# Optimization experiments

Hardware: AMD Instinct MI355X
Metric: run time of the kernel (lower is better)

Reference implementation:

```python
import jax, jax.numpy as jnp
import numpy as np

B, S, F, H = 64, 1024, 64, 128


def setup_inputs() -> dict:
    key = jax.random.key(0)
    ks = jax.random.split(key, 12)
    s = 1.0 / np.sqrt(H)
    u = lambda k, shape: jax.random.uniform(k, shape, jnp.float32, -s, s)
    return {
        "x": jax.random.normal(ks[0], (B, S, F), jnp.float32),
        "mu": jax.random.normal(ks[1], (B, 1, F), jnp.float32),
        "W_ih0": u(ks[2], (4 * H, F)),
        "W_hh0": u(ks[3], (4 * H, H)),
        "b_ih0": u(ks[4], (4 * H,)),
        "b_hh0": u(ks[5], (4 * H,)),
        "W_ih1": u(ks[6], (4 * H, H)),
        "W_hh1": u(ks[7], (4 * H, H)),
        "b_ih1": u(ks[8], (4 * H,)),
        "b_hh1": u(ks[9], (4 * H,)),
        "fc_w": u(ks[10], (1, H)),
        "fc_b": u(ks[11], (1,)),
    }


def _cell(x_gates, h, c, Whh, bias):
    # PyTorch LSTM cell: gates ordered i, f, g, o
    g = x_gates + h @ Whh.T + bias
    i, f, gg, o = jnp.split(g, 4, axis=-1)
    c = jax.nn.sigmoid(f) * c + jax.nn.sigmoid(i) * jnp.tanh(gg)
    h = jax.nn.sigmoid(o) * jnp.tanh(c)
    return h, c


def _lstm2(x1, x2, Wih, Whh, bih, bhh):
    # 2-step LSTM layer from zero initial state; returns per-step hidden states
    bias = bih + bhh
    n = x1.shape[0]
    hd = Whh.shape[1]
    h0 = jnp.zeros((n, hd), x1.dtype)
    h1, c1 = _cell(x1 @ Wih.T, h0, h0, Whh, bias)
    h2, _ = _cell(x2 @ Wih.T, h1, c1, Whh, bias)
    return h1, h2


def reference(x, mu, W_ih0, W_hh0, b_ih0, b_hh0, W_ih1, W_hh1, b_ih1, b_hh1, fc_w, fc_b):
    b, s, f = x.shape
    # Every timestep runs an independent 2-step LSTM [x_t, mu] from zero state,
    # so fold (batch, seq) into one big batch of B*S instances.
    x1 = x.reshape(b * s, f)                                   # step-1 inputs
    x2 = jnp.broadcast_to(mu, (b, s, f)).reshape(b * s, f)     # step-2 inputs (mu)
    h1, h2 = _lstm2(x1, x2, W_ih0, W_hh0, b_ih0, b_hh0)        # layer 0
    _, h2 = _lstm2(h1, h2, W_ih1, W_hh1, b_ih1, b_hh1)         # layer 1
    h = jax.nn.relu(h2).reshape(b, s, -1)                      # relu; dropout is identity (eval)
    out = h @ fc_w.T + fc_b                                    # [B, S, 1]
    return out
```

## Files before the change

### kernel.cpp

```cpp
#include <hip/hip_runtime.h>


typedef _Float16 half8 __attribute__((ext_vector_type(8)));
typedef _Float16 half4_t __attribute__((ext_vector_type(4)));
typedef float f32x4 __attribute__((ext_vector_type(4)));

#define L2E  1.4426950408889634f
#define L2E2 2.8853900817779268f

#define WP_WIH0 0
#define WP_WHH0 32768
#define WP_WIH1 98304
#define WP_WHH1 163840
#define WS_BIAS0 458752
#define WS_BIAS1 (458752 + 2048)
#define WS_MUG2  (458752 + 4096)

__global__ void prep_kernel(const float* __restrict__ Wih0,
                            const float* __restrict__ Whh0,
                            const float* __restrict__ Wih1,
                            const float* __restrict__ Whh1,
                            const float* __restrict__ bih0,
                            const float* __restrict__ bhh0,
                            const float* __restrict__ bih1,
                            const float* __restrict__ bhh1,
                            const float* __restrict__ mu,
                            _Float16* __restrict__ Wp,
                            float* __restrict__ bias0f,
                            float* __restrict__ bias1f,
                            float* __restrict__ mu_g2)
{
    int blk = blockIdx.x;
    if (blk >= 113) {
        int o = (blk - 113) * 256 + threadIdx.x;
        int b = o >> 9;
        int n = o & 511;
        float s = bih0[n] + bhh0[n];
        const float* m = mu + b * 64;
        const float* wrow = Wih0 + n * 64;
        #pragma unroll 8
        for (int k = 0; k < 64; ++k) s += m[k] * wrow[k];
        float scale = ((n >> 7) == 2) ? L2E2 : L2E;
        mu_g2[o] = s * scale;
        return;
    }
    if (blk == 112) {
        int i = threadIdx.x;
        float sc_hi = (i < 128) ? L2E2 : L2E;
        bias0f[i]       = (bih0[i]       + bhh0[i])       * L2E;
        bias0f[i + 256] = (bih0[i + 256] + bhh0[i + 256]) * sc_hi;
        bias1f[i]       = (bih1[i]       + bhh1[i])       * L2E;
        bias1f[i + 256] = (bih1[i + 256] + bhh1[i + 256]) * sc_hi;
        return;
    }
    int gidx = blk * 256 + threadIdx.x;
    const float* src; int KC, Kw, local;
    if (gidx < 4096)       { src = Wih0; KC = 2; Kw = 64;  local = gidx; }
    else if (gidx < 12288) { src = Whh0; KC = 4; Kw = 128; local = gidx - 4096; }
    else if (gidx < 20480) { src = Wih1; KC = 4; Kw = 128; local = gidx - 12288; }
    else                   { src = Whh1; KC = 4; Kw = 128; local = gidx - 20480; }
    int lane = local & 63;
    int tmp  = local >> 6;
    int kc   = tmp % KC;
    int nt   = tmp / KC;
    int n  = nt * 16 + (lane & 15);
    int k0 = kc * 32 + (lane >> 4) * 8;
    float scale = ((n >> 7) == 2) ? L2E2 : L2E;
    const float* s = src + n * Kw + k0;
    half8 hv;
    #pragma unroll
    for (int j = 0; j < 8; ++j) hv[j] = (_Float16)(s[j] * scale);
    *(half8*)(Wp + (size_t)gidx * 8) = hv;
}

__device__ __forceinline__ float sig2(float a) {
    return __builtin_amdgcn_rcpf(1.0f + __builtin_amdgcn_exp2f(-a));
}
__device__ __forceinline__ float tanh2(float a) {
    return fmaf(-2.0f, __builtin_amdgcn_rcpf(1.0f + __builtin_amdgcn_exp2f(a)), 1.0f);
}

__device__ __forceinline__ int swz(int row, int col) {
    return (row << 8) + (col ^ ((row & 7) << 4));
}

template<int KC>
__device__ __forceinline__ void gemm_stage(const _Float16* __restrict__ Wq,
                                           const _Float16* A, const int strideA,
                                           int w, int lane, f32x4 acc[4][4])
{
    const int c = lane & 15, q = lane >> 4;
    #pragma unroll
    for (int kc = 0; kc < KC; ++kc) {
        half8 a[4], bq[4];
        #pragma unroll
        for (int mt = 0; mt < 4; ++mt)
            a[mt] = *(const half8*)(A + (mt * 16 + c) * strideA + kc * 32 + q * 8);
        #pragma unroll
        for (int g = 0; g < 4; ++g)
            bq[g] = *(const half8*)(Wq + (((g * 8 + w) * KC + kc) * 64 + lane) * 8);
        #pragma unroll
        for (int mt = 0; mt < 4; ++mt)
            #pragma unroll
            for (int g = 0; g < 4; ++g)
                acc[mt][g] = __builtin_amdgcn_mfma_f32_16x16x32_f16(bq[g], a[mt], acc[mt][g], 0, 0, 0);
    }
}

template<int KC>
__device__ __forceinline__ void gemm_lds(const _Float16* __restrict__ Wq,
                                         const char* Hb,
                                         int w, int lane, f32x4 acc[4][4])
{
    const int c = lane & 15, q = lane >> 4;
    #pragma unroll
    for (int kc = 0; kc < KC; ++kc) {
        half8 a[4], bq[4];
        #pragma unroll
        for (int mt = 0; mt < 4; ++mt)
            a[mt] = *(const half8*)(Hb + swz(mt * 16 + c, kc * 64 + q * 16));
        #pragma unroll
        for (int g = 0; g < 4; ++g)
            bq[g] = *(const half8*)(Wq + (((g * 8 + w) * KC + kc) * 64 + lane) * 8);
        #pragma unroll
        for (int mt = 0; mt < 4; ++mt)
            #pragma unroll
            for (int g = 0; g < 4; ++g)
                acc[mt][g] = __builtin_amdgcn_mfma_f32_16x16x32_f16(bq[g], a[mt], acc[mt][g], 0, 0, 0);
    }
}

__global__ __launch_bounds__(512) void lstm_main(
    const float* __restrict__ x, const _Float16* __restrict__ Wp_in,
    const float* __restrict__ bias0f_in, const float* __restrict__ bias1f_in,
    const float* __restrict__ mu_g2_in, const float* __restrict__ fc_w_in,
    const float* __restrict__ fc_b_in, float* __restrict__ out)
{
    __shared__ __align__(16) char smem[58368];
    char* H1s  = smem;
    char* H2s  = smem + 16384;
    char* H11s = smem + 32768;
    _Float16* A0 = (_Float16*)(smem + 49152);

    const int t = threadIdx.x;
    const int w = t >> 6, lane = t & 63, c = lane & 15, q = lane >> 4;
    const int wg = blockIdx.x;
    const int b = wg >> 4;
    const int bq_idx = w * 4 + q;

    {
        const float* xp = x + (size_t)wg * 4096 + t * 8;
        float4 u0 = ((const float4*)xp)[0];
        float4 u1 = ((const float4*)xp)[1];
        half8 hv;
        hv[0] = (_Float16)u0.x; hv[1] = (_Float16)u0.y;
        hv[2] = (_Float16)u0.z; hv[3] = (_Float16)u0.w;
        hv[4] = (_Float16)u1.x; hv[5] = (_Float16)u1.y;
        hv[6] = (_Float16)u1.z; hv[7] = (_Float16)u1.w;
        *(half8*)(A0 + (t >> 3) * 72 + (t & 7) * 8) = hv;
        if (t < 64) out[(size_t)wg * 64 + t] = fc_b_in[0];
    }
    __syncthreads();

    f32x4 acc[4][4];
    float cc[4][4];

    {
        const float* bias0f = bias0f_in; asm volatile("" : "+s"(bias0f));
        #pragma unroll
        for (int g = 0; g < 4; ++g) {
            f32x4 bv = ((const f32x4*)bias0f)[g * 32 + bq_idx];
            #pragma unroll
            for (int mt = 0; mt < 4; ++mt) acc[mt][g] = bv;
        }
    }
    {
        const _Float16* W0 = Wp_in + WP_WIH0; asm volatile("" : "+s"(W0));
        __builtin_amdgcn_s_setprio(1);
        gemm_stage<2>(W0, A0, 72, w, lane, acc);
        __builtin_amdgcn_s_setprio(0);
    }
    #pragma unroll
    for (int mt = 0; mt < 4; ++mt) {
        half4_t hv;
        #pragma unroll
        for (int r = 0; r < 4; ++r) {
            float c1 = sig2(acc[mt][0][r]) * tanh2(acc[mt][2][r]);
            cc[mt][r] = c1;
            hv[r] = (_Float16)(sig2(acc[mt][3][r]) * tanh2(c1 * L2E2));
        }
        *(half4_t*)(H1s + swz(mt * 16 + c, w * 32 + q * 8)) = hv;
    }
    __syncthreads();

    {
        const float* mu_g2b = mu_g2_in + b * 512; asm volatile("" : "+s"(mu_g2b));
        #pragma unroll
        for (int g = 0; g < 4; ++g) {
            f32x4 bv = ((const f32x4*)mu_g2b)[g * 32 + bq_idx];
            #pragma unroll
            for (int mt = 0; mt < 4; ++mt) acc[mt][g] = bv;
        }
    }
    {
        const _Float16* Wq = Wp_in + WP_WHH0; asm volatile("" : "+s"(Wq));
        __builtin_amdgcn_s_setprio(1);
        gemm_lds<4>(Wq, H1s, w, lane, acc);
        __builtin_amdgcn_s_setprio(0);
    }

    f32x4 bv1[4];
    {
        const float* bias1f = bias1f_in; asm volatile("" : "+s"(bias1f));
        #pragma unroll
        for (int g = 0; g < 4; ++g)
            bv1[g] = ((const f32x4*)bias1f)[g * 32 + bq_idx];
    }

    {
        const _Float16* Wih1p = Wp_in + WP_WIH1; asm volatile("" : "+s"(Wih1p));
        #pragma unroll
        for (int mt = 0; mt < 4; ++mt) {
            half4_t hv;
            #pragma unroll
            for (int r = 0; r < 4; ++r) {
                float c2 = sig2(acc[mt][1][r]) * cc[mt][r]
                         + sig2(acc[mt][0][r]) * tanh2(acc[mt][2][r]);
                hv[r] = (_Float16)(sig2(acc[mt][3][r]) * tanh2(c2 * L2E2));
            }
            *(half4_t*)(H2s + swz(mt * 16 + c, w * 32 + q * 8)) = hv;
            #pragma unroll
            for (int g = 0; g < 4; ++g) acc[mt][g] = bv1[g];
            __builtin_amdgcn_s_setprio(1);
            #pragma unroll
            for (int kc = 0; kc < 4; ++kc) {
                half8 av = *(const half8*)(H1s + swz(mt * 16 + c, kc * 64 + q * 16));
                #pragma unroll
                for (int g = 0; g < 4; ++g) {
                    half8 bq = *(const half8*)(Wih1p + (((g * 8 + w) * 4 + kc) * 64 + lane) * 8);
                    acc[mt][g] = __builtin_amdgcn_mfma_f32_16x16x32_f16(bq, av, acc[mt][g], 0, 0, 0);
                }
            }
            __builtin_amdgcn_s_setprio(0);
        }
    }
    #pragma unroll
    for (int mt = 0; mt < 4; ++mt) {
        half4_t hv;
        #pragma unroll
        for (int r = 0; r < 4; ++r) {
            float c1 = sig2(acc[mt][0][r]) * tanh2(acc[mt][2][r]);
            cc[mt][r] = c1;
            hv[r] = (_Float16)(sig2(acc[mt][3][r]) * tanh2(c1 * L2E2));
        }
        *(half4_t*)(H11s + swz(mt * 16 + c, w * 32 + q * 8)) = hv;
    }
    __syncthreads();

    #pragma unroll
    for (int g = 0; g < 4; ++g)
        #pragma unroll
        for (int mt = 0; mt < 4; ++mt) acc[mt][g] = bv1[g];
    {
        const _Float16* Wa = Wp_in + WP_WIH1; asm volatile("" : "+s"(Wa));
        const _Float16* Wb = Wp_in + WP_WHH1; asm volatile("" : "+s"(Wb));
        __builtin_amdgcn_s_setprio(1);
        gemm_lds<4>(Wa, H2s,  w, lane, acc);
        gemm_lds<4>(Wb, H11s, w, lane, acc);
        __builtin_amdgcn_s_setprio(0);
    }
    {
        const float* fc_w = fc_w_in; asm volatile("" : "+s"(fc_w));
        f32x4 fwv = ((const f32x4*)fc_w)[bq_idx];
        #pragma unroll
        for (int mt = 0; mt < 4; ++mt) {
            float v = 0.0f;
            #pragma unroll
            for (int r = 0; r < 4; ++r) {
                float c2 = sig2(acc[mt][1][r]) * cc[mt][r]
                         + sig2(acc[mt][0][r]) * tanh2(acc[mt][2][r]);
                float h  = sig2(acc[mt][3][r]) * tanh2(c2 * L2E2);
                v = fmaf(fmaxf(h, 0.0f), fwv[r], v);
            }
            v += __shfl_xor(v, 16);
            v += __shfl_xor(v, 32);
            if (lane < 16)
                atomicAdd(out + (size_t)wg * 64 + mt * 16 + lane, v);
        }
    }
}

extern "C" void kernel_launch(void* const* d_in, const int* in_sizes, int n_in,
                              void* d_out, int out_size, void* d_ws, size_t ws_size,
                              hipStream_t stream)
{
    const float* x    = (const float*)d_in[0];
    const float* mu   = (const float*)d_in[1];
    const float* Wih0 = (const float*)d_in[2];
    const float* Whh0 = (const float*)d_in[3];
    const float* bih0 = (const float*)d_in[4];
    const float* bhh0 = (const float*)d_in[5];
    const float* Wih1 = (const float*)d_in[6];
    const float* Whh1 = (const float*)d_in[7];
    const float* bih1 = (const float*)d_in[8];
    const float* bhh1 = (const float*)d_in[9];
    const float* fcw  = (const float*)d_in[10];
    const float* fcb  = (const float*)d_in[11];
    float* out = (float*)d_out;

    _Float16* Wp  = (_Float16*)d_ws;
    float* bias0f = (float*)((char*)d_ws + WS_BIAS0);
    float* bias1f = (float*)((char*)d_ws + WS_BIAS1);
    float* mu_g2  = (float*)((char*)d_ws + WS_MUG2);

    hipLaunchKernelGGL(prep_kernel, dim3(241), dim3(256), 0, stream,
                       Wih0, Whh0, Wih1, Whh1, bih0, bhh0, bih1, bhh1, mu,
                       Wp, bias0f, bias1f, mu_g2);
    hipLaunchKernelGGL(lstm_main, dim3(1024), dim3(512), 0, stream,
                       x, Wp, bias0f, bias1f, mu_g2, fcw, fcb, out);
}
```

Measured before the change: 144.7 us.

## Software-pipeline weight fragment loads across GEMM stages with lighter barriers

Merges the GEMM helpers into one routine that prefetches the next k-chunk's weight fragments into registers while the current MFMAs run, carrying the prefetch into the next stage's weights. It folds bias initialisation into the first MFMA's accumulator input and swaps __syncthreads for an LDS-only wait plus s_barrier. The layer-1 step-1 GEMM is moved out of the per-mt interleaving with the layer-0 activation write, so H2s is fully written before Wih1·H1 runs. These changes aim to hide global/L2 weight-load latency, at the cost of extra live registers that could lower occupancy or cause spills.

Result: faster. 134.7 us (-6.9%).

```diff
diff --git a/kernel.cpp b/kernel.cpp
--- a/kernel.cpp
+++ b/kernel.cpp
@@ -84,49 +84,60 @@
     return (row << 8) + (col ^ ((row & 7) << 4));
 }
 
-template<int KC>
-__device__ __forceinline__ void gemm_stage(const _Float16* __restrict__ Wq,
-                                           const _Float16* A, const int strideA,
-                                           int w, int lane, f32x4 acc[4][4])
+__device__ __forceinline__ void lds_barrier() {
+    asm volatile("s_waitcnt lgkmcnt(0)" ::: "memory");
+    __builtin_amdgcn_s_barrier();
+    asm volatile("" ::: "memory");
+}
+
+__device__ __forceinline__ void load_bq(half8 bq[4], const _Float16* __restrict__ Wq,
+                                        int KC, int kc, int w, int lane)
+{
+    #pragma unroll
+    for (int g = 0; g < 4; ++g)
+        bq[g] = *(const half8*)(Wq + (((g * 8 + w) * KC + kc) * 64 + lane) * 8);
+}
+
+template<int SRC>
+__device__ __forceinline__ void load_a(half8 a[4], const char* base, int kc, int c, int q)
+{
+    #pragma unroll
+    for (int mt = 0; mt < 4; ++mt) {
+        if (SRC == 0)
+            a[mt] = *(const half8*)((const _Float16*)base + (mt * 16 + c) * 72 + kc * 32 + q * 8);
+        else
+            a[mt] = *(const half8*)(base + swz(mt * 16 + c, kc * 64 + q * 16));
+    }
+}
+
+template<int KC, int SRC, bool PF, bool FIRST>
+__device__ __forceinline__ void gemm_pf(const _Float16* __restrict__ Wq,
+                                        const char* Abase,
+                                        const _Float16* __restrict__ Wnext, int KCnext,
+                                        half8 bqc[4], const f32x4 bv[4],
+                                        int w, int lane, f32x4 acc[4][4])
 {
     const int c = lane & 15, q = lane >> 4;
     #pragma unroll
     for (int kc = 0; kc < KC; ++kc) {
-        half8 a[4], bq[4];
+        half8 bqn[4];
+        if (kc + 1 < KC)  load_bq(bqn, Wq, KC, kc + 1, w, lane);
+        else if (PF)      load_bq(bqn, Wnext, KCnext, 0, w, lane);
+        half8 a[4];
+        load_a<SRC>(a, Abase, kc, c, q);
+        __builtin_amdgcn_s_setprio(1);
         #pragma unroll
         for (int mt = 0; mt < 4; ++mt)
-            a[mt] = *(const half8*)(A + (mt * 16 + c) * strideA + kc * 32 + q * 8);
-        #pragma unroll
-        for (int g = 0; g < 4; ++g)
-            bq[g] = *(const half8*)(Wq + (((g * 8 + w) * KC + kc) * 64 + lane) * 8);
-        #pragma unroll
-        for (int mt = 0; mt < 4; ++mt)
-            #pragma unroll
-            for (int g = 0; g < 4; ++g)
-                acc[mt][g] = __builtin_amdgcn_mfma_f32_16x16x32_f16(bq[g], a[mt], acc[mt][g], 0, 0, 0);
-    }
-}
-
-template<int KC>
-__device__ __forceinline__ void gemm_lds(const _Float16* __restrict__ Wq,
-                                         const char* Hb,
-                                         int w, int lane, f32x4 acc[4][4])
-{
-    const int c = lane & 15, q = lane >> 4;
-    #pragma unroll
-    for (int kc = 0; kc < KC; ++kc) {
-        half8 a[4], bq[4];
-        #pragma unroll
-        for (int mt = 0; mt < 4; ++mt)
-            a[mt] = *(const half8*)(Hb + swz(mt * 16 + c, kc * 64 + q * 16));
-        #pragma unroll
-        for (int g = 0; g < 4; ++g)
-            bq[g] = *(const half8*)(Wq + (((g * 8 + w) * KC + kc) * 64 + lane) * 8);
-        #pragma unroll
-        for (int mt = 0; mt < 4; ++mt)
-            #pragma unroll
-            for (int g = 0; g < 4; ++g)
-                acc[mt][g] = __builtin_amdgcn_mfma_f32_16x16x32_f16(bq[g], a[mt], acc[mt][g], 0, 0, 0);
+            #pragma unroll
+            for (int g = 0; g < 4; ++g) {
+                f32x4 cin = (FIRST && kc == 0) ? bv[g] : acc[mt][g];
+                acc[mt][g] = __builtin_amdgcn_mfma_f32_16x16x32_f16(bqc[g], a[mt], cin, 0, 0, 0);
+            }
+        __builtin_amdgcn_s_setprio(0);
+        if (kc + 1 < KC || PF) {
+            #pragma unroll
+            for (int g = 0; g < 4; ++g) bqc[g] = bqn[g];
+        }
     }
 }
 
@@ -147,6 +158,9 @@
     const int wg = blockIdx.x;
     const int b = wg >> 4;
     const int bq_idx = w * 4 + q;
+
+    half8 bqc[4];
+    load_bq(bqc, Wp_in + WP_WIH0, 2, 0, w, lane);
 
     {
         const float* xp = x + (size_t)wg * 4096 + t * 8;
@@ -160,25 +174,21 @@
         *(half8*)(A0 + (t >> 3) * 72 + (t & 7) * 8) = hv;
         if (t < 64) out[(size_t)wg * 64 + t] = fc_b_in[0];
     }
-    __syncthreads();
+    lds_barrier();
 
     f32x4 acc[4][4];
     float cc[4][4];
 
     {
-        const float* bias0f = bias0f_in; asm volatile("" : "+s"(bias0f));
-        #pragma unroll
-        for (int g = 0; g < 4; ++g) {
-            f32x4 bv = ((const f32x4*)bias0f)[g * 32 + bq_idx];
-            #pragma unroll
-            for (int mt = 0; mt < 4; ++mt) acc[mt][g] = bv;
-        }
-    }
-    {
-        const _Float16* W0 = Wp_in + WP_WIH0; asm volatile("" : "+s"(W0));
-        __builtin_amdgcn_s_setprio(1);
-        gemm_stage<2>(W0, A0, 72, w, lane, acc);
-        __builtin_amdgcn_s_setprio(0);
+        f32x4 bv[4];
+        {
+            const float* bias0f = bias0f_in; asm volatile("" : "+s"(bias0f));
+            #pragma unroll
+            for (int g = 0; g < 4; ++g)
+                bv[g] = ((const f32x4*)bias0f)[g * 32 + bq_idx];
+        }
+        gemm_pf<2, 0, true, true>(Wp_in + WP_WIH0, (const char*)A0,
+                                  Wp_in + WP_WHH0, 4, bqc, bv, w, lane, acc);
     }
     #pragma unroll
     for (int mt = 0; mt < 4; ++mt) {
@@ -191,58 +201,41 @@
         }
         *(half4_t*)(H1s + swz(mt * 16 + c, w * 32 + q * 8)) = hv;
     }
-    __syncthreads();
-
-    {
-        const float* mu_g2b = mu_g2_in + b * 512; asm volatile("" : "+s"(mu_g2b));
-        #pragma unroll
-        for (int g = 0; g < 4; ++g) {
-            f32x4 bv = ((const f32x4*)mu_g2b)[g * 32 + bq_idx];
-            #pragma unroll
-            for (int mt = 0; mt < 4; ++mt) acc[mt][g] = bv;
-        }
-    }
-    {
-        const _Float16* Wq = Wp_in + WP_WHH0; asm volatile("" : "+s"(Wq));
-        __builtin_amdgcn_s_setprio(1);
-        gemm_lds<4>(Wq, H1s, w, lane, acc);
-        __builtin_amdgcn_s_setprio(0);
-    }
-
-    f32x4 bv1[4];
-    {
-        const float* bias1f = bias1f_in; asm volatile("" : "+s"(bias1f));
-        #pragma unroll
-        for (int g = 0; g < 4; ++g)
-            bv1[g] = ((const f32x4*)bias1f)[g * 32 + bq_idx];
-    }
-
-    {
-        const _Float16* Wih1p = Wp_in + WP_WIH1; asm volatile("" : "+s"(Wih1p));
-        #pragma unroll
-        for (int mt = 0; mt < 4; ++mt) {
-            half4_t hv;
-            #pragma unroll
-            for (int r = 0; r < 4; ++r) {
-                float c2 = sig2(acc[mt][1][r]) * cc[mt][r]
-                         + sig2(acc[mt][0][r]) * tanh2(acc[mt][2][r]);
-                hv[r] = (_Float16)(sig2(acc[mt][3][r]) * tanh2(c2 * L2E2));
-            }
-            *(half4_t*)(H2s + swz(mt * 16 + c, w * 32 + q * 8)) = hv;
-            #pragma unroll
-            for (int g = 0; g < 4; ++g) acc[mt][g] = bv1[g];
-            __builtin_amdgcn_s_setprio(1);
-            #pragma unroll
-            for (int kc = 0; kc < 4; ++kc) {
-                half8 av = *(const half8*)(H1s + swz(mt * 16 + c, kc * 64 + q * 16));
-                #pragma unroll
-                for (int g = 0; g < 4; ++g) {
-                    half8 bq = *(const half8*)(Wih1p + (((g * 8 + w) * 4 + kc) * 64 + lane) * 8);
-                    acc[mt][g] = __builtin_amdgcn_mfma_f32_16x16x32_f16(bq, av, acc[mt][g], 0, 0, 0);
-                }
-            }
-            __builtin_amdgcn_s_setprio(0);
-        }
+    lds_barrier();
+
+    {
+        f32x4 bv[4];
+        {
+            const float* mu_g2b = mu_g2_in + b * 512; asm volatile("" : "+s"(mu_g2b));
+            #pragma unroll
+            for (int g = 0; g < 4; ++g)
+                bv[g] = ((const f32x4*)mu_g2b)[g * 32 + bq_idx];
+        }
+        gemm_pf<4, 1, true, true>(Wp_in + WP_WHH0, H1s,
+                                  Wp_in + WP_WIH1, 4, bqc, bv, w, lane, acc);
+    }
+    #pragma unroll
+    for (int mt = 0; mt < 4; ++mt) {
+        half4_t hv;
+        #pragma unroll
+        for (int r = 0; r < 4; ++r) {
+            float c2 = sig2(acc[mt][1][r]) * cc[mt][r]
+                     + sig2(acc[mt][0][r]) * tanh2(acc[mt][2][r]);
+            hv[r] = (_Float16)(sig2(acc[mt][3][r]) * tanh2(c2 * L2E2));
+        }
+        *(half4_t*)(H2s + swz(mt * 16 + c, w * 32 + q * 8)) = hv;
+    }
+
+    {
+        f32x4 bv[4];
+        {
+            const float* bias1f = bias1f_in; asm volatile("" : "+s"(bias1f));
+            #pragma unroll
+            for (int g = 0; g < 4; ++g)
+                bv[g] = ((const f32x4*)bias1f)[g * 32 + bq_idx];
+        }
+        gemm_pf<4, 1, true, true>(Wp_in + WP_WIH1, H1s,
+                                  Wp_in + WP_WIH1, 4, bqc, bv, w, lane, acc);
     }
     #pragma unroll
     for (int mt = 0; mt < 4; ++mt) {
@@ -255,20 +248,22 @@
         }
         *(half4_t*)(H11s + swz(mt * 16 + c, w * 32 + q * 8)) = hv;
     }
-    __syncthreads();
-
-    #pragma unroll
-    for (int g = 0; g < 4; ++g)
-        #pragma unroll
-        for (int mt = 0; mt < 4; ++mt) acc[mt][g] = bv1[g];
-    {
-        const _Float16* Wa = Wp_in + WP_WIH1; asm volatile("" : "+s"(Wa));
-        const _Float16* Wb = Wp_in + WP_WHH1; asm volatile("" : "+s"(Wb));
-        __builtin_amdgcn_s_setprio(1);
-        gemm_lds<4>(Wa, H2s,  w, lane, acc);
-        gemm_lds<4>(Wb, H11s, w, lane, acc);
-        __builtin_amdgcn_s_setprio(0);
-    }
+    lds_barrier();
+
+    {
+        f32x4 bv[4];
+        {
+            const float* bias1f = bias1f_in; asm volatile("" : "+s"(bias1f));
+            #pragma unroll
+            for (int g = 0; g < 4; ++g)
+                bv[g] = ((const f32x4*)bias1f)[g * 32 + bq_idx];
+        }
+        gemm_pf<4, 1, true, true>(Wp_in + WP_WIH1, H2s,
+                                  Wp_in + WP_WHH1, 4, bqc, bv, w, lane, acc);
+    }
+    gemm_pf<4, 1, false, false>(Wp_in + WP_WHH1, H11s,
+                                nullptr, 0, bqc, nullptr, w, lane, acc);
+
     {
         const float* fc_w = fc_w_in; asm volatile("" : "+s"(fc_w));
         f32x4 fwv = ((const f32x4*)fc_w)[bq_idx];
```
